# Kernel tuning notes

Hardware: AMD Instinct MI355X
Metric: run time of the kernel (lower is better)

Reference implementation:

```python
import jax, jax.numpy as jnp
import numpy as np

N, M, D = 8192, 8192, 64

def setup_inputs() -> dict:
    key = jax.random.key(0)
    kx, ky = jax.random.split(key)
    x = jax.random.normal(kx, (N, D), dtype=jnp.float32)
    y = jax.random.normal(ky, (M, D), dtype=jnp.float32)
    sigma = jnp.array(1.0, dtype=jnp.float32)
    return {"x": x, "y": y, "sigma": sigma}

def reference(x, y, sigma):
    # Flatten trailing dims (no-op here since inputs are already 2-D).
    x2 = x.reshape(x.shape[0], -1)
    y2 = y.reshape(y.shape[0], -1)
    # Pairwise squared distances via the GEMM trick:
    # |x_i - y_j|^2 = |x_i|^2 + |y_j|^2 - 2 x_i . y_j
    xn = jnp.sum(x2 * x2, axis=1)            # [N]
    yn = jnp.sum(y2 * y2, axis=1)            # [M]
    cross = x2 @ y2.T                         # [N, M]
    sqd = xn[:, None] + yn[None, :] - 2.0 * cross
    sqd = jnp.maximum(sqd, 0.0)               # clamp tiny negatives from fp error
    return jnp.exp(-0.5 * sqd / (sigma * sigma))  # [N, M]
```

## Files before the change

### kernel.cpp

```cpp
#include <hip/hip_runtime.h>
#include <hip/hip_bf16.h>

#define N 8192
#define M 8192
#define D 64

typedef __bf16 bf16x8 __attribute__((ext_vector_type(8)));
typedef float f32x4 __attribute__((ext_vector_type(4)));

__global__ __launch_bounds__(256) void prep_kernel(
    const float* __restrict__ x, const float* __restrict__ y,
    __bf16* __restrict__ xh, __bf16* __restrict__ xl, float* __restrict__ xn,
    __bf16* __restrict__ yh, __bf16* __restrict__ yl, float* __restrict__ yn)
{
    int row  = blockIdx.x * 4 + (threadIdx.x >> 6);
    int lane = threadIdx.x & 63;

    const float* src;
    __bf16 *h, *l;
    float* nrm;
    int r;
    if (row < N) { src = x; h = xh; l = xl; nrm = xn; r = row; }
    else         { src = y; h = yh; l = yl; nrm = yn; r = row - N; }

    float v = src[(size_t)r * D + lane];
    __bf16 hi = (__bf16)v;
    float  lof = v - (float)hi;
    __bf16 lo = (__bf16)lof;

    h[(size_t)r * D + lane] = hi;
    l[(size_t)r * D + lane] = lo;

    float s = v * v;
    #pragma unroll
    for (int off = 32; off; off >>= 1) s += __shfl_down(s, off, 64);
    if (lane == 0) nrm[r] = s;
}

__global__ __launch_bounds__(256) void rbf_kernel(
    const __bf16* __restrict__ xh, const __bf16* __restrict__ xl,
    const float* __restrict__ xn,
    const __bf16* __restrict__ yh, const __bf16* __restrict__ yl,
    const float* __restrict__ yn,
    const float* __restrict__ sig, float* __restrict__ out)
{
    int tid  = threadIdx.x;
    int wave = tid >> 6;
    int lane = tid & 63;
    int quad = lane >> 4;
    int l16  = lane & 15;

    int i_base = blockIdx.y * 128 + (wave >> 1) * 64;
    int j_base = blockIdx.x * 128 + (wave & 1) * 64;

    float s = sig[0];
    float scale = -0.5f / (s * s);

    bf16x8 Ah[4][2], Al[4][2];
    #pragma unroll
    for (int ti = 0; ti < 4; ++ti) {
        int row = i_base + ti * 16 + l16;
        #pragma unroll
        for (int k = 0; k < 2; ++k) {
            int off = row * D + k * 32 + quad * 8;
            Ah[ti][k] = *reinterpret_cast<const bf16x8*>(xh + off);
            Al[ti][k] = *reinterpret_cast<const bf16x8*>(xl + off);
        }
    }

    float xnr[4][4];
    #pragma unroll
    for (int ti = 0; ti < 4; ++ti)
        #pragma unroll
        for (int r = 0; r < 4; ++r)
            xnr[ti][r] = xn[i_base + ti * 16 + quad * 4 + r];

    #pragma unroll
    for (int tj = 0; tj < 4; ++tj) {
        int col = j_base + tj * 16 + l16;

        bf16x8 Bh[2], Bl[2];
        #pragma unroll
        for (int k = 0; k < 2; ++k) {
            int off = col * D + k * 32 + quad * 8;
            Bh[k] = *reinterpret_cast<const bf16x8*>(yh + off);
            Bl[k] = *reinterpret_cast<const bf16x8*>(yl + off);
        }
        float ynj = yn[col];

        f32x4 acc[4];
        #pragma unroll
        for (int ti = 0; ti < 4; ++ti) acc[ti] = (f32x4){0.f, 0.f, 0.f, 0.f};

        #pragma unroll
        for (int ti = 0; ti < 4; ++ti) {
            #pragma unroll
            for (int k = 0; k < 2; ++k) {
                acc[ti] = __builtin_amdgcn_mfma_f32_16x16x32_bf16(Ah[ti][k], Bh[k], acc[ti], 0, 0, 0);
                acc[ti] = __builtin_amdgcn_mfma_f32_16x16x32_bf16(Ah[ti][k], Bl[k], acc[ti], 0, 0, 0);
                acc[ti] = __builtin_amdgcn_mfma_f32_16x16x32_bf16(Al[ti][k], Bh[k], acc[ti], 0, 0, 0);
            }
        }

        #pragma unroll
        for (int ti = 0; ti < 4; ++ti) {
            #pragma unroll
            for (int r = 0; r < 4; ++r) {
                int row = i_base + ti * 16 + quad * 4 + r;
                float sqd = xnr[ti][r] + ynj - 2.0f * acc[ti][r];
                sqd = fmaxf(sqd, 0.0f);
                out[(size_t)row * M + col] = __expf(scale * sqd);
            }
        }
    }
}

extern "C" void kernel_launch(void* const* d_in, const int* in_sizes, int n_in,
                              void* d_out, int out_size, void* d_ws, size_t ws_size,
                              hipStream_t stream) {
    const float* x   = (const float*)d_in[0];
    const float* y   = (const float*)d_in[1];
    const float* sig = (const float*)d_in[2];
    float* out = (float*)d_out;

    char* ws = (char*)d_ws;
    __bf16* xh = (__bf16*)(ws);
    __bf16* xl = (__bf16*)(ws + (1u << 20));
    __bf16* yh = (__bf16*)(ws + (2u << 20));
    __bf16* yl = (__bf16*)(ws + (3u << 20));
    float*  xn = (float*) (ws + (4u << 20));
    float*  yn = (float*) (ws + (4u << 20) + (1u << 15));

    prep_kernel<<<(N + M) / 4, 256, 0, stream>>>(x, y, xh, xl, xn, yh, yl, yn);

    dim3 grid(M / 128, N / 128);
    rbf_kernel<<<grid, 256, 0, stream>>>(xh, xl, xn, yh, yl, yn, sig, out);
}
```

Before: 309.7 us.

## Permute column mapping so each lane stores contiguous float4 output

Each lane now owns four consecutive output columns: B fragments are loaded for columns 4*l16+t, and the four 16-column tiles are interleaved. This lets every output row be written as a single 16-byte vector store instead of four scalar stores. Y stays resident in registers while X fragments are streamed per row tile. The output write is the dominant cost of this kernel, so wider stores should cut store instruction count and improve coalescing.

```diff
diff --git a/kernel.cpp b/kernel.cpp
--- a/kernel.cpp
+++ b/kernel.cpp
@@ -56,61 +56,61 @@
     float s = sig[0];
     float scale = -0.5f / (s * s);
 
-    bf16x8 Ah[4][2], Al[4][2];
+    bf16x8 Bh[4][2], Bl[4][2];
+    float ynr[4];
     #pragma unroll
-    for (int ti = 0; ti < 4; ++ti) {
-        int row = i_base + ti * 16 + l16;
+    for (int t = 0; t < 4; ++t) {
+        int col = j_base + 4 * l16 + t;
+        ynr[t] = yn[col];
         #pragma unroll
         for (int k = 0; k < 2; ++k) {
-            int off = row * D + k * 32 + quad * 8;
-            Ah[ti][k] = *reinterpret_cast<const bf16x8*>(xh + off);
-            Al[ti][k] = *reinterpret_cast<const bf16x8*>(xl + off);
+            int off = col * D + k * 32 + quad * 8;
+            Bh[t][k] = *reinterpret_cast<const bf16x8*>(yh + off);
+            Bl[t][k] = *reinterpret_cast<const bf16x8*>(yl + off);
         }
     }
 
-    float xnr[4][4];
     #pragma unroll
-    for (int ti = 0; ti < 4; ++ti)
+    for (int ti = 0; ti < 4; ++ti) {
+        int arow = i_base + ti * 16 + l16;
+        bf16x8 Ah[2], Al[2];
+        #pragma unroll
+        for (int k = 0; k < 2; ++k) {
+            int off = arow * D + k * 32 + quad * 8;
+            Ah[k] = *reinterpret_cast<const bf16x8*>(xh + off);
+            Al[k] = *reinterpret_cast<const bf16x8*>(xl + off);
+        }
+
+        float xnr[4];
         #pragma unroll
         for (int r = 0; r < 4; ++r)
-            xnr[ti][r] = xn[i_base + ti * 16 + quad * 4 + r];
-
-    #pragma unroll
-    for (int tj = 0; tj < 4; ++tj) {
-        int col = j_base + tj * 16 + l16;
-
-        bf16x8 Bh[2], Bl[2];
-        #pragma unroll
-        for (int k = 0; k < 2; ++k) {
-            int off = col * D + k * 32 + quad * 8;
-            Bh[k] = *reinterpret_cast<const bf16x8*>(yh + off);
-            Bl[k] = *reinterpret_cast<const bf16x8*>(yl + off);
-        }
-        float ynj = yn[col];
+            xnr[r] = xn[i_base + ti * 16 + quad * 4 + r];
 
         f32x4 acc[4];
         #pragma unroll
-        for (int ti = 0; ti < 4; ++ti) acc[ti] = (f32x4){0.f, 0.f, 0.f, 0.f};
+        for (int t = 0; t < 4; ++t) acc[t] = (f32x4){0.f, 0.f, 0.f, 0.f};
 
         #pragma unroll
-        for (int ti = 0; ti < 4; ++ti) {
+        for (int t = 0; t < 4; ++t) {
             #pragma unroll
             for (int k = 0; k < 2; ++k) {
-                acc[ti] = __builtin_amdgcn_mfma_f32_16x16x32_bf16(Ah[ti][k], Bh[k], acc[ti], 0, 0, 0);
-                acc[ti] = __builtin_amdgcn_mfma_f32_16x16x32_bf16(Ah[ti][k], Bl[k], acc[ti], 0, 0, 0);
-                acc[ti] = __builtin_amdgcn_mfma_f32_16x16x32_bf16(Al[ti][k], Bh[k], acc[ti], 0, 0, 0);
+                acc[t] = __builtin_amdgcn_mfma_f32_16x16x32_bf16(Ah[k], Bh[t][k], acc[t], 0, 0, 0);
+                acc[t] = __builtin_amdgcn_mfma_f32_16x16x32_bf16(Ah[k], Bl[t][k], acc[t], 0, 0, 0);
+                acc[t] = __builtin_amdgcn_mfma_f32_16x16x32_bf16(Al[k], Bh[t][k], acc[t], 0, 0, 0);
             }
         }
 
         #pragma unroll
-        for (int ti = 0; ti < 4; ++ti) {
+        for (int r = 0; r < 4; ++r) {
+            int row = i_base + ti * 16 + quad * 4 + r;
+            f32x4 v;
             #pragma unroll
-            for (int r = 0; r < 4; ++r) {
-                int row = i_base + ti * 16 + quad * 4 + r;
-                float sqd = xnr[ti][r] + ynj - 2.0f * acc[ti][r];
+            for (int t = 0; t < 4; ++t) {
+                float sqd = xnr[r] + ynr[t] - 2.0f * acc[t][r];
                 sqd = fmaxf(sqd, 0.0f);
-                out[(size_t)row * M + col] = __expf(scale * sqd);
+                v[t] = __expf(scale * sqd);
             }
+            *reinterpret_cast<f32x4*>(out + (size_t)row * M + j_base + 4 * l16) = v;
         }
     }
 }
```

After: 291.2 us. 6.0% less time.
